# Kernel optimization log

Hardware: AMD Instinct MI355X
Metric: run time of the kernel (lower is better)

## Reference

```python
import jax, jax.numpy as jnp
import numpy as np

NEVENTS = 100000
EMB_DIM = 64
NCONDS = 50
BATCH = 16384


def setup_inputs() -> dict:
    key = jax.random.key(0)
    k_idx, k_tab = jax.random.split(key)
    inp = jax.random.randint(k_idx, (BATCH, 1 + NCONDS), 0, NEVENTS + 2, dtype=jnp.int64 if jax.config.jax_enable_x64 else jnp.int32)
    event_table = jax.random.normal(k_tab, (NEVENTS + 2, EMB_DIM), dtype=jnp.float32)
    return {"input": inp, "event_table": event_table}


def reference(input, event_table):
    # Note: original module defines cond_embedding but uses event_embedding for both lookups.
    event = input[:, 0:1]          # [B, 1]
    conditions = input[:, 1:]      # [B, C]
    event_emb = event_table[event]        # [B, 1, D]
    cond_emb = event_table[conditions]    # [B, C, D]
    # L2 normalize along last dim (torch .norm(dim=2, keepdim=True))
    event_nrm = event_emb / jnp.linalg.norm(event_emb, axis=2, keepdims=True)
    cond_nrm = cond_emb / jnp.linalg.norm(cond_emb, axis=2, keepdims=True)
    # scores: [B, 1, C] = event_nrm @ cond_nrm^T
    scores = jnp.einsum('bod,bcd->boc', event_nrm, cond_nrm)
    # filtered_cond: [B, C, D] = cond_nrm * scores.transpose(1,2) (broadcast over D)
    filtered_cond = cond_nrm * jnp.swapaxes(scores, 1, 2)
    B = input.shape[0]
    return jnp.concatenate((event_emb.reshape(B, -1), filtered_cond.reshape(B, -1)), axis=1)
```

## Files before the change

kernel.cpp:

```cpp
#include <hip/hip_runtime.h>

#define NCONDS 50
#define EMB 64
#define ROW_STRIDE (1 + NCONDS)
#define OUT_STRIDE ((1 + NCONDS) * EMB)
#define NITER 13

typedef float f4 __attribute__((ext_vector_type(4)));

template<int CTRL>
__device__ __forceinline__ float dpp_add(float x) {
    int y = __builtin_amdgcn_update_dpp(0, __builtin_bit_cast(int, x),
                                        CTRL, 0xf, 0xf, true);
    return x + __builtin_bit_cast(float, y);
}
__device__ __forceinline__ float reduce16(float x) {
    x = dpp_add<0x121>(x);
    x = dpp_add<0x122>(x);
    x = dpp_add<0x124>(x);
    x = dpp_add<0x128>(x);
    return x;
}

__global__ __launch_bounds__(256) void cond_filter_kernel(
    const int*   __restrict__ inp,
    const float* __restrict__ table,
    float*       __restrict__ out,
    int batch)
{
    const int wave = threadIdx.x >> 6;
    const int lane = threadIdx.x & 63;
    int b = blockIdx.x * 4 + wave;
    b = __builtin_amdgcn_readfirstlane(b);
    if (b >= batch) return;

    const int grp = lane >> 4;
    const int gl  = lane & 15;

    const int* row = inp + (size_t)b * ROW_STRIDE;
    const int e_idx = row[0];

    int cidx[NITER];
    #pragma unroll
    for (int i = 0; i < NITER; ++i) {
        const int base = 1 + i * 4;
        const int s0 = row[base];
        const int s1 = (base + 1 < ROW_STRIDE) ? row[base + 1] : s0;
        const int s2 = (base + 2 < ROW_STRIDE) ? row[base + 2] : s0;
        const int s3 = (base + 3 < ROW_STRIDE) ? row[base + 3] : s0;
        cidx[i] = (grp & 1) ? ((grp & 2) ? s3 : s1)
                            : ((grp & 2) ? s2 : s0);
    }

    const f4 ev = *(const f4*)(table + (size_t)e_idx * EMB + gl * 4);
    f4 cv[NITER];
    #pragma unroll
    for (int i = 0; i < NITER; ++i)
        cv[i] = *(const f4*)(table + (size_t)cidx[i] * EMB + gl * 4);

    const float es = reduce16(ev.x*ev.x + ev.y*ev.y + ev.z*ev.z + ev.w*ev.w);
    const float e_rn = rsqrtf(es);
    const f4 en = ev * e_rn;

    float* orow = out + (size_t)b * OUT_STRIDE;
    if (grp == 0) {
        __builtin_nontemporal_store(ev, (f4*)(orow + gl * 4));
    }

    #pragma unroll
    for (int i = 0; i < NITER; ++i) {
        const int c = i * 4 + grp;
        const f4 v = cv[i];
        const float cs = reduce16(v.x*v.x + v.y*v.y + v.z*v.z + v.w*v.w);
        const float dp = reduce16(v.x*en.x + v.y*en.y + v.z*en.z + v.w*en.w);
        const float scale = dp * __builtin_amdgcn_rcpf(cs);
        if (c < NCONDS) {
            const f4 o = v * scale;
            __builtin_nontemporal_store(o, (f4*)(orow + EMB + (size_t)c * EMB + gl * 4));
        }
    }
}

extern "C" void kernel_launch(void* const* d_in, const int* in_sizes, int n_in,
                              void* d_out, int out_size, void* d_ws, size_t ws_size,
                              hipStream_t stream) {
    const int*   inp   = (const int*)d_in[0];
    const float* table = (const float*)d_in[1];
    float*       out   = (float*)d_out;

    const int batch = in_sizes[0] / ROW_STRIDE;
    const int blocks = (batch + 3) / 4;

    hipLaunchKernelGGL(cond_filter_kernel, dim3(blocks), dim3(256), 0, stream,
                       inp, table, out, batch);
}
```

Baseline: 249.8 us.

## Partition table lookups into index slices across blocks for cache locality

Each row block is now handled by 8 blocks, and each of those processes only the condition indices that fall into its slice of the embedding table. The intent is to keep each block's working set of the 25.6MB table small enough to be cache-resident. Matching indices are compacted through shared memory using a ballot, and the next row's indices are prefetched. The cost is that every slice block re-reads the indices and recomputes the event normalization. The per-row compaction loop is serial, which lowers memory-level parallelism compared with issuing all 13 gathers at once.

New measurement: 287.1 us. +14.9%, slower.

```diff
diff --git a/kernel.cpp b/kernel.cpp
--- a/kernel.cpp
+++ b/kernel.cpp
@@ -4,7 +4,10 @@
 #define EMB 64
 #define ROW_STRIDE (1 + NCONDS)
 #define OUT_STRIDE ((1 + NCONDS) * EMB)
-#define NITER 13
+#define NSLICE 8
+#define SLICE_ROWS 12501u
+#define ROWS_PER_BLOCK 64
+#define ROWS_PER_WAVE 16
 
 typedef float f4 __attribute__((ext_vector_type(4)));
 
@@ -22,62 +25,84 @@
     return x;
 }
 
-__global__ __launch_bounds__(256) void cond_filter_kernel(
+__device__ __forceinline__ int slice_of(int idx) {
+    return (int)((unsigned)idx / SLICE_ROWS);
+}
+
+__global__ __launch_bounds__(256) void cond_filter_sliced(
     const int*   __restrict__ inp,
     const float* __restrict__ table,
     float*       __restrict__ out,
     int batch)
 {
-    const int wave = threadIdx.x >> 6;
+    __shared__ int cl[4][64];
+
+    const int wv   = threadIdx.x >> 6;
     const int lane = threadIdx.x & 63;
-    int b = blockIdx.x * 4 + wave;
-    b = __builtin_amdgcn_readfirstlane(b);
-    if (b >= batch) return;
+    const int grp  = lane >> 4;
+    const int gl   = lane & 15;
 
-    const int grp = lane >> 4;
-    const int gl  = lane & 15;
+    const int slice  = blockIdx.x & (NSLICE - 1);
+    const int rowblk = blockIdx.x >> 3;
+    int rbase = rowblk * ROWS_PER_BLOCK + wv * ROWS_PER_WAVE;
+    rbase = __builtin_amdgcn_readfirstlane(rbase);
 
-    const int* row = inp + (size_t)b * ROW_STRIDE;
-    const int e_idx = row[0];
+    if (rbase >= batch) return;
 
-    int cidx[NITER];
-    #pragma unroll
-    for (int i = 0; i < NITER; ++i) {
-        const int base = 1 + i * 4;
-        const int s0 = row[base];
-        const int s1 = (base + 1 < ROW_STRIDE) ? row[base + 1] : s0;
-        const int s2 = (base + 2 < ROW_STRIDE) ? row[base + 2] : s0;
-        const int s3 = (base + 3 < ROW_STRIDE) ? row[base + 3] : s0;
-        cidx[i] = (grp & 1) ? ((grp & 2) ? s3 : s1)
-                            : ((grp & 2) ? s2 : s0);
-    }
+    const int* row0 = inp + (size_t)rbase * ROW_STRIDE;
+    int e_idx = row0[0];
+    int ci = (lane < NCONDS) ? __builtin_nontemporal_load(row0 + 1 + lane) : 0;
 
-    const f4 ev = *(const f4*)(table + (size_t)e_idx * EMB + gl * 4);
-    f4 cv[NITER];
-    #pragma unroll
-    for (int i = 0; i < NITER; ++i)
-        cv[i] = *(const f4*)(table + (size_t)cidx[i] * EMB + gl * 4);
+    for (int rr = 0; rr < ROWS_PER_WAVE; ++rr) {
+        const int b = rbase + rr;
+        if (b >= batch) return;
 
-    const float es = reduce16(ev.x*ev.x + ev.y*ev.y + ev.z*ev.z + ev.w*ev.w);
-    const float e_rn = rsqrtf(es);
-    const f4 en = ev * e_rn;
+        int e_nx = 0, ci_nx = 0;
+        if (rr + 1 < ROWS_PER_WAVE && b + 1 < batch) {
+            const int* nrow = inp + (size_t)(b + 1) * ROW_STRIDE;
+            e_nx  = nrow[0];
+            ci_nx = (lane < NCONDS) ? __builtin_nontemporal_load(nrow + 1 + lane) : 0;
+        }
 
-    float* orow = out + (size_t)b * OUT_STRIDE;
-    if (grp == 0) {
-        __builtin_nontemporal_store(ev, (f4*)(orow + gl * 4));
-    }
+        float* orow = out + (size_t)b * OUT_STRIDE;
 
-    #pragma unroll
-    for (int i = 0; i < NITER; ++i) {
-        const int c = i * 4 + grp;
-        const f4 v = cv[i];
-        const float cs = reduce16(v.x*v.x + v.y*v.y + v.z*v.z + v.w*v.w);
-        const float dp = reduce16(v.x*en.x + v.y*en.y + v.z*en.z + v.w*en.w);
-        const float scale = dp * __builtin_amdgcn_rcpf(cs);
-        if (c < NCONDS) {
-            const f4 o = v * scale;
-            __builtin_nontemporal_store(o, (f4*)(orow + EMB + (size_t)c * EMB + gl * 4));
+        const f4 ev = __builtin_nontemporal_load(
+            (const f4*)(table + (size_t)e_idx * EMB + gl * 4));
+        const float es = reduce16(ev.x*ev.x + ev.y*ev.y + ev.z*ev.z + ev.w*ev.w);
+        const f4 en = ev * rsqrtf(es);
+
+        if ((slice_of(e_idx) == slice) && grp == 0)
+            __builtin_nontemporal_store(ev, (f4*)(orow + gl * 4));
+
+        const bool match = (lane < NCONDS) && (slice_of(ci) == slice);
+        const unsigned long long m = __ballot(match);
+        const int cnt = __popcll(m);
+
+        if (cnt > 0) {
+            if (match) {
+                const int pos = __popcll(m & ((1ull << lane) - 1));
+                cl[wv][pos] = (ci << 6) | lane;
+            }
+            const int nt = (cnt + 3) >> 2;
+            for (int t = 0; t < nt; ++t) {
+                const int e  = t * 4 + grp;
+                const int pk = cl[wv][e < cnt ? e : cnt - 1];
+                const int c   = pk & 63;
+                const int idx = pk >> 6;
+                const f4 v = *(const f4*)(table + (size_t)idx * EMB + gl * 4);
+                const float cs = reduce16(v.x*v.x + v.y*v.y + v.z*v.z + v.w*v.w);
+                const float dp = reduce16(v.x*en.x + v.y*en.y + v.z*en.z + v.w*en.w);
+                const float scale = dp * __builtin_amdgcn_rcpf(cs);
+                if (e < cnt) {
+                    const f4 o = v * scale;
+                    __builtin_nontemporal_store(o,
+                        (f4*)(orow + EMB + (size_t)c * EMB + gl * 4));
+                }
+            }
         }
+
+        e_idx = e_nx;
+        ci    = ci_nx;
     }
 }
 
@@ -88,9 +113,10 @@
     const float* table = (const float*)d_in[1];
     float*       out   = (float*)d_out;
 
-    const int batch = in_sizes[0] / ROW_STRIDE;
-    const int blocks = (batch + 3) / 4;
+    const int batch   = in_sizes[0] / ROW_STRIDE;
+    const int rowblks = (batch + ROWS_PER_BLOCK - 1) / ROWS_PER_BLOCK;
+    const int blocks  = rowblks * NSLICE;
 
-    hipLaunchKernelGGL(cond_filter_kernel, dim3(blocks), dim3(256), 0, stream,
+    hipLaunchKernelGGL(cond_filter_sliced, dim3(blocks), dim3(256), 0, stream,
                        inp, table, out, batch);
 }
```

## Bin condition lookups by table slice and process them in a second pass

Applied to the files above, without the earlier changes.

Splits the work into two kernels. The first writes the raw event embeddings, stores normalized event vectors to a workspace, and buckets every (condition index, row, slot) tuple into 8 bins by table row range. The second processes each bin so that gathers from the embedding table hit a narrower address range, aiming for better cache locality. In exchange it adds an extra pass over the bin and normalized-event buffers, global atomics, and scattered 256-byte output writes. It falls back to the original kernel when the workspace is too small.

New measurement: 285.6 us. 14.3% more time.

```diff
diff --git a/kernel.cpp b/kernel.cpp
--- a/kernel.cpp
+++ b/kernel.cpp
@@ -2,11 +2,16 @@
 
 #define NCONDS 50
 #define EMB 64
-#define ROW_STRIDE (1 + NCONDS)
+#define ROW_STRIDE 51
 #define OUT_STRIDE ((1 + NCONDS) * EMB)
 #define NITER 13
+#define NSLICE 8
+#define SLICE_ROWS 12501u
+#define BIN_CAP 131072
+#define P1_ROWS 64
 
 typedef float f4 __attribute__((ext_vector_type(4)));
+typedef unsigned long long u64;
 
 template<int CTRL>
 __device__ __forceinline__ float dpp_add(float x) {
@@ -20,6 +25,131 @@
     x = dpp_add<0x124>(x);
     x = dpp_add<0x128>(x);
     return x;
+}
+
+__global__ __launch_bounds__(256) void p1_bin(
+    const int*   __restrict__ inp,
+    const float* __restrict__ table,
+    float*       __restrict__ out,
+    float*       __restrict__ enbuf,
+    u64*         __restrict__ bins,
+    unsigned*    __restrict__ gcnt,
+    int batch)
+{
+    __shared__ int      stash[P1_ROWS][ROW_STRIDE];
+    __shared__ unsigned lcnt[NSLICE];
+    __shared__ unsigned loff[NSLICE];
+
+    const int wv   = threadIdx.x >> 6;
+    const int lane = threadIdx.x & 63;
+    const int grp  = lane >> 4;
+    const int gl   = lane & 15;
+    const int rbase = blockIdx.x * P1_ROWS;
+
+    if (threadIdx.x < NSLICE) lcnt[threadIdx.x] = 0;
+    __syncthreads();
+
+    for (int r = wv; r < P1_ROWS; r += 4) {
+        const int R = rbase + r;
+        if (R >= batch) break;
+        int ci = 0;
+        if (lane < ROW_STRIDE) {
+            ci = inp[(size_t)R * ROW_STRIDE + lane];
+            stash[r][lane] = ci;
+        }
+        const int e_idx = __shfl(ci, 0);
+        const f4 ev = *(const f4*)(table + (size_t)e_idx * EMB + gl * 4);
+        const float es = reduce16(ev.x*ev.x + ev.y*ev.y + ev.z*ev.z + ev.w*ev.w);
+        const f4 en = ev * rsqrtf(es);
+        if (grp == 0) {
+            *(f4*)(enbuf + (size_t)R * EMB + gl * 4) = en;
+            __builtin_nontemporal_store(ev, (f4*)(out + (size_t)R * OUT_STRIDE + gl * 4));
+        }
+        const bool valid = (lane >= 1) && (lane <= NCONDS);
+        const int  sl    = (int)((unsigned)ci / SLICE_ROWS);
+        #pragma unroll
+        for (int s = 0; s < NSLICE; ++s) {
+            const u64 m = __ballot(valid && (sl == s));
+            if (lane == s && m) atomicAdd(&lcnt[s], (unsigned)__popcll(m));
+        }
+    }
+    __syncthreads();
+
+    if (threadIdx.x < NSLICE)
+        loff[threadIdx.x] = atomicAdd(&gcnt[threadIdx.x], lcnt[threadIdx.x]);
+    __syncthreads();
+
+    for (int r = wv; r < P1_ROWS; r += 4) {
+        const int R = rbase + r;
+        if (R >= batch) break;
+        if (lane >= 1 && lane <= NCONDS) {
+            const int ci = stash[r][lane];
+            const int sl = (int)((unsigned)ci / SLICE_ROWS);
+            const unsigned pos = atomicAdd(&loff[sl], 1u);
+            if (pos < BIN_CAP)
+                bins[(size_t)sl * BIN_CAP + pos] =
+                    ((u64)(unsigned)ci << 32) | (unsigned)((R << 6) | (lane - 1));
+        }
+    }
+}
+
+__global__ __launch_bounds__(256) void p2_filter(
+    const float*    __restrict__ table,
+    const float*    __restrict__ enbuf,
+    const u64*      __restrict__ bins,
+    const unsigned* __restrict__ gcnt,
+    float*          __restrict__ out)
+{
+    const int wv   = threadIdx.x >> 6;
+    const int lane = threadIdx.x & 63;
+    const int grp  = lane >> 4;
+    const int gl   = lane & 15;
+    const int s    = blockIdx.x & (NSLICE - 1);
+    const int w    = (blockIdx.x >> 3) * 4 + wv;
+
+    unsigned count = gcnt[s];
+    if (count > BIN_CAP) count = BIN_CAP;
+    count = __builtin_amdgcn_readfirstlane(count);
+    const unsigned per   = (count + 511) >> 9;
+    const unsigned start = (unsigned)w * per;
+    unsigned end = start + per;
+    if (end > count) end = count;
+    if (start >= end) return;
+
+    const u64* bs = bins + (size_t)s * BIN_CAP;
+
+    for (unsigned e0 = start; e0 < end; e0 += 32) {
+        u64 ent[8];
+        f4  v[8], en[8];
+        #pragma unroll
+        for (int r = 0; r < 8; ++r) {
+            const unsigned e = e0 + r * 4 + grp;
+            ent[r] = bs[e < end ? e : end - 1];
+        }
+        #pragma unroll
+        for (int r = 0; r < 8; ++r) {
+            const unsigned idx = (unsigned)(ent[r] >> 32);
+            const unsigned b   = ((unsigned)ent[r] & 0xFFFFFu) >> 6;
+            v[r]  = *(const f4*)(table + (size_t)idx * EMB + gl * 4);
+            en[r] = *(const f4*)(enbuf + (size_t)b   * EMB + gl * 4);
+        }
+        #pragma unroll
+        for (int r = 0; r < 8; ++r) {
+            const unsigned bc = (unsigned)ent[r] & 0xFFFFFu;
+            const unsigned b  = bc >> 6;
+            const unsigned c  = bc & 63u;
+            const f4 vv = v[r], ee = en[r];
+            const float cs = reduce16(vv.x*vv.x + vv.y*vv.y + vv.z*vv.z + vv.w*vv.w);
+            const float dp = reduce16(vv.x*ee.x + vv.y*ee.y + vv.z*ee.z + vv.w*ee.w);
+            const float scale = dp * __builtin_amdgcn_rcpf(cs);
+            const unsigned e = e0 + r * 4 + grp;
+            if (e < end) {
+                const f4 o = vv * scale;
+                __builtin_nontemporal_store(o,
+                    (f4*)(out + (size_t)b * OUT_STRIDE + EMB + (size_t)c * EMB + gl * 4));
+            }
+        }
+    }
 }
 
 __global__ __launch_bounds__(256) void cond_filter_kernel(
@@ -59,13 +189,11 @@
         cv[i] = *(const f4*)(table + (size_t)cidx[i] * EMB + gl * 4);
 
     const float es = reduce16(ev.x*ev.x + ev.y*ev.y + ev.z*ev.z + ev.w*ev.w);
-    const float e_rn = rsqrtf(es);
-    const f4 en = ev * e_rn;
+    const f4 en = ev * rsqrtf(es);
 
     float* orow = out + (size_t)b * OUT_STRIDE;
-    if (grp == 0) {
+    if (grp == 0)
         __builtin_nontemporal_store(ev, (f4*)(orow + gl * 4));
-    }
 
     #pragma unroll
     for (int i = 0; i < NITER; ++i) {
@@ -89,8 +217,26 @@
     float*       out   = (float*)d_out;
 
     const int batch = in_sizes[0] / ROW_STRIDE;
-    const int blocks = (batch + 3) / 4;
-
-    hipLaunchKernelGGL(cond_filter_kernel, dim3(blocks), dim3(256), 0, stream,
-                       inp, table, out, batch);
-}
+
+    const size_t bins_bytes = (size_t)NSLICE * BIN_CAP * sizeof(u64);
+    const size_t en_bytes   = (size_t)batch * EMB * sizeof(float);
+    const size_t need       = 256 + bins_bytes + en_bytes;
+
+    if (d_ws != nullptr && ws_size >= need) {
+        unsigned* gcnt  = (unsigned*)d_ws;
+        u64*      bins  = (u64*)((char*)d_ws + 256);
+        float*    enbuf = (float*)((char*)d_ws + 256 + bins_bytes);
+
+        hipMemsetAsync(gcnt, 0, 64, stream);
+
+        const int blocks1 = (batch + P1_ROWS - 1) / P1_ROWS;
+        hipLaunchKernelGGL(p1_bin, dim3(blocks1), dim3(256), 0, stream,
+                           inp, table, out, enbuf, bins, gcnt, batch);
+        hipLaunchKernelGGL(p2_filter, dim3(1024), dim3(256), 0, stream,
+                           table, enbuf, bins, gcnt, out);
+    } else {
+        const int blocks = (batch + 3) / 4;
+        hipLaunchKernelGGL(cond_filter_kernel, dim3(blocks), dim3(256), 0, stream,
+                           inp, table, out, batch);
+    }
+}
```
